# Kernel optimization log

Hardware: AMD Instinct MI355X
Metric: run time of the kernel (lower is better)

Reference implementation:

```python
import jax, jax.numpy as jnp
import numpy as np

B, T, W = 128, 256, 256
D, C, K = 128, 256, 12
TEMP = 0.1


def _l2norm(x):
    # matches F.normalize(dim=-1, eps=1e-12)
    return x / jnp.maximum(jnp.linalg.norm(x, axis=-1, keepdims=True), 1e-12)


def setup_inputs() -> dict:
    key = jax.random.key(0)
    ks = jax.random.split(key, 12)
    s = 0.02
    return {
        "rr_windows": jax.random.normal(ks[0], (B, T, W), dtype=jnp.float32),
        # Encoder: 2-layer MLP window->2D->D
        "enc_w1": jax.random.normal(ks[1], (W, 2 * D), dtype=jnp.float32) * s,
        "enc_b1": jnp.zeros((2 * D,), dtype=jnp.float32),
        "enc_w2": jax.random.normal(ks[2], (2 * D, D), dtype=jnp.float32) * s,
        "enc_b2": jnp.zeros((D,), dtype=jnp.float32),
        # ARBlock: single-layer GRU latent->context
        "W_ih": jax.random.normal(ks[3], (3 * C, D), dtype=jnp.float32) * s,
        "W_hh": jax.random.normal(ks[4], (3 * C, C), dtype=jnp.float32) * s,
        "b_ih": jnp.zeros((3 * C,), dtype=jnp.float32),
        "b_hh": jnp.zeros((3 * C,), dtype=jnp.float32),
        # K prediction heads Wk: context->latent
        "Wk_w": jax.random.normal(ks[5], (K, C, D), dtype=jnp.float32) * s,
        "Wk_b": jnp.zeros((K, D), dtype=jnp.float32),
    }


def _gru(z_seq, W_ih, W_hh, b_ih, b_hh):
    # z_seq: [B, T, D] -> c_seq [B, T, C]
    gx = jnp.einsum("btd,gd->btg", z_seq, W_ih) + b_ih  # [B,T,3C]
    gx = jnp.swapaxes(gx, 0, 1)  # [T,B,3C]
    h0 = jnp.zeros((z_seq.shape[0], C), dtype=z_seq.dtype)

    def step(h, gx_t):
        gh = h @ W_hh.T + b_hh
        xr, xz, xn = jnp.split(gx_t, 3, axis=-1)
        hr, hz, hn = jnp.split(gh, 3, axis=-1)
        r = jax.nn.sigmoid(xr + hr)
        zg = jax.nn.sigmoid(xz + hz)
        n = jnp.tanh(xn + r * hn)
        h_new = (1.0 - zg) * n + zg * h
        return h_new, h_new

    _, hs = jax.lax.scan(step, h0, gx)  # [T,B,C]
    return jnp.swapaxes(hs, 0, 1)


def reference(rr_windows, enc_w1, enc_b1, enc_w2, enc_b2, W_ih, W_hh, b_ih, b_hh, Wk_w, Wk_b):
    # Encoder on each window (dropout inactive)
    h = jax.nn.relu(jnp.einsum("btw,wh->bth", rr_windows, enc_w1) + enc_b1)
    z_seq = jnp.einsum("bth,hd->btd", h, enc_w2) + enc_b2  # [B,T,D]
    z_seq = _l2norm(z_seq)
    c_seq = _gru(z_seq, W_ih, W_hh, b_ih, b_hh)  # [B,T,C]

    Tp = T - K
    c_used = c_seq[:, :Tp, :]  # [B,Tp,C]
    # all (t,k) predictions at once: [K,B,Tp,D]
    preds = _l2norm(jnp.einsum("btc,kcd->kbtd", c_used, Wk_w) + Wk_b[:, None, None, :])
    # logits over ALL timesteps; cat([pos, negs-excl-pos]) == full set reordered,
    # so cross_entropy = logsumexp(full) - pos_logit (logsumexp order-invariant)
    logits = jnp.einsum("kbtd,bsd->kbts", preds, z_seq) / TEMP  # [K,B,Tp,T]
    pos_idx = jnp.arange(Tp)[None, :] + jnp.arange(1, K + 1)[:, None]  # [K,Tp]
    pos_logit = jnp.take_along_axis(
        logits, pos_idx[:, None, :, None], axis=-1
    )[..., 0]  # [K,B,Tp]
    avg_loss = jnp.mean(jax.nn.logsumexp(logits, axis=-1) - pos_logit)

    # accuracy: positive beats all negatives (ties to positive, as in argmax w/ pos first)
    is_pos = jnp.arange(T)[None, None, None, :] == pos_idx[:, None, :, None]
    neg_max = jnp.max(jnp.where(is_pos, -jnp.inf, logits), axis=-1)
    avg_accuracy = jnp.mean((pos_logit >= neg_max).astype(jnp.float32)) * 100.0
    return (avg_loss, avg_accuracy, z_seq, c_seq)
```

## Files before the change

### kernel.cpp

```cpp
#include <hip/hip_runtime.h>
#include <stdint.h>


typedef _Float16 f16;
typedef __attribute__((ext_vector_type(2))) _Float16 f16x2;
typedef __attribute__((ext_vector_type(8))) _Float16 f16x8;
typedef __attribute__((ext_vector_type(4))) float f32x4;

__device__ __forceinline__ f16x2 u2h(unsigned int x) { return __builtin_bit_cast(f16x2, x); }
__device__ __forceinline__ float sigm_(float x) { return __builtin_amdgcn_rcpf(1.f + __expf(-x)); }
__device__ __forceinline__ float tanh_(float x) { return 1.f - 2.f * __builtin_amdgcn_rcpf(__expf(2.f * x) + 1.f); }

#define NTOT_LOSS 374784.0f

__global__ void k_prep(const float* __restrict__ w1, const float* __restrict__ w2,
                       const float* __restrict__ wih, const float* __restrict__ whh,
                       const float* __restrict__ wkw,
                       f16* __restrict__ w1T, f16* __restrict__ w2T, f16* __restrict__ wihF,
                       uint8_t* __restrict__ whhQ, float* __restrict__ wsc,
                       f16* __restrict__ wkT, float* __restrict__ accb) {
  const int stride = gridDim.x * blockDim.x;
  const int tid = blockIdx.x * blockDim.x + threadIdx.x;
  if (tid == 0) { accb[0] = 0.f; accb[1] = 0.f; }
  for (int i = tid; i < 65536; i += stride) { int n = i >> 8, k = i & 255; w1T[i] = (f16)w1[k * 256 + n]; }
  for (int i = tid; i < 32768; i += stride) { int n = i >> 8, k = i & 255; w2T[i] = (f16)w2[k * 128 + n]; }
  for (int i = tid; i < 98304; i += stride) wihF[i] = (f16)wih[i];
  if (tid < 768) {
    const float* row = whh + (size_t)tid * 256;
    float amax = 0.f;
    for (int k = 0; k < 256; ++k) amax = fmaxf(amax, fabsf(row[k]));
    const float s = fmaxf(amax, 1e-20f) / 127.f;
    const float rs = 127.f / fmaxf(amax, 1e-20f);
    wsc[tid] = s / 127.f;
    for (int jq = 0; jq < 16; ++jq) {
      uint32_t words[4];
      for (int w32 = 0; w32 < 4; ++w32) {
        uint32_t p = 0;
        for (int e = 0; e < 4; ++e) {
          const int k = jq * 16 + w32 * 4 + e;
          const int q = (int)rintf(row[k] * rs);
          p |= ((uint32_t)(uint8_t)(int8_t)q) << (8 * e);
        }
        words[w32] = p;
      }
      *(uint4*)(whhQ + ((size_t)jq * 768 + tid) * 16) =
          make_uint4(words[0], words[1], words[2], words[3]);
    }
  }
  for (int i = tid; i < 393216; i += stride) {
    int kk = i >> 15, rem = i & 32767, d = rem >> 8, c = rem & 255;
    wkT[i] = (f16)wkw[(kk << 15) + c * 128 + d];
  }
}

template <int KTOT, bool AF32, bool RELU>
__global__ __launch_bounds__(256) void k_gemm64(const void* __restrict__ Aptr,
                                                const f16* __restrict__ BT,
                                                const float* __restrict__ bias,
                                                f16* __restrict__ out, const int NT) {
  __shared__ __align__(16) f16 Al[64][40];
  __shared__ __align__(16) f16 Bl[64][40];
  const int m0 = blockIdx.x * 64;
  const int n0 = blockIdx.y * 64;
  const int t = threadIdx.x;
  const int w = t >> 6, l = t & 63, lr = l & 15, lg = l >> 4;
  const int arow = t >> 2, akq = (t & 3) * 8;
  f32x4 acc[4] = {};
  for (int ks = 0; ks < KTOT / 32; ++ks) {
    const int kc = ks * 32;
    __syncthreads();
    if constexpr (AF32) {
      const float* src = (const float*)Aptr + (size_t)(m0 + arow) * KTOT + kc + akq;
      float4 v0 = *(const float4*)src;
      float4 v1 = *(const float4*)(src + 4);
      f16x8 hv = {(f16)v0.x, (f16)v0.y, (f16)v0.z, (f16)v0.w,
                  (f16)v1.x, (f16)v1.y, (f16)v1.z, (f16)v1.w};
      *(f16x8*)&Al[arow][akq] = hv;
    } else {
      const f16* src = (const f16*)Aptr + (size_t)(m0 + arow) * KTOT + kc + akq;
      *(f16x8*)&Al[arow][akq] = *(const f16x8*)src;
    }
    *(f16x8*)&Bl[arow][akq] = *(const f16x8*)(BT + (size_t)(n0 + arow) * KTOT + kc + akq);
    __syncthreads();
    f16x8 af = *(const f16x8*)&Al[16 * w + lr][lg * 8];
#pragma unroll
    for (int nt = 0; nt < 4; ++nt) {
      f16x8 bf = *(const f16x8*)&Bl[nt * 16 + lr][lg * 8];
      acc[nt] = __builtin_amdgcn_mfma_f32_16x16x32_f16(af, bf, acc[nt], 0, 0, 0);
    }
  }
#pragma unroll
  for (int nt = 0; nt < 4; ++nt) {
    const int n = n0 + nt * 16 + lr;
    const float bb = bias[n];
#pragma unroll
    for (int r = 0; r < 4; ++r) {
      const int m = m0 + 16 * w + lg * 4 + r;
      float v = acc[nt][r] + bb;
      if (RELU) v = fmaxf(v, 0.f);
      out[(size_t)m * NT + n] = (f16)v;
    }
  }
}

__global__ __launch_bounds__(256) void k_enc2(const f16* __restrict__ A, const f16* __restrict__ BT,
                                              const float* __restrict__ bias,
                                              float* __restrict__ zf32, f16* __restrict__ zf16) {
  __shared__ __align__(16) f16 Al[64][40];
  __shared__ __align__(16) f16 Bl[128][40];
  const int m0 = blockIdx.x * 64;
  const int t = threadIdx.x;
  const int w = t >> 6, l = t & 63, lr = l & 15, lg = l >> 4;
  const int arow = t >> 2, akq = (t & 3) * 8;
  f32x4 acc[8] = {};
  for (int ks = 0; ks < 8; ++ks) {
    const int kc = ks * 32;
    __syncthreads();
    *(f16x8*)&Al[arow][akq] = *(const f16x8*)(A + (size_t)(m0 + arow) * 256 + kc + akq);
#pragma unroll
    for (int hh = 0; hh < 2; ++hh) {
      const int brow = arow + 64 * hh;
      *(f16x8*)&Bl[brow][akq] = *(const f16x8*)(BT + (size_t)brow * 256 + kc + akq);
    }
    __syncthreads();
    f16x8 af = *(const f16x8*)&Al[16 * w + lr][lg * 8];
#pragma unroll
    for (int nt = 0; nt < 8; ++nt) {
      f16x8 bf = *(const f16x8*)&Bl[nt * 16 + lr][lg * 8];
      acc[nt] = __builtin_amdgcn_mfma_f32_16x16x32_f16(af, bf, acc[nt], 0, 0, 0);
    }
  }
  float v[8][4];
#pragma unroll
  for (int nt = 0; nt < 8; ++nt) {
    const float bb = bias[nt * 16 + lr];
#pragma unroll
    for (int r = 0; r < 4; ++r) v[nt][r] = acc[nt][r] + bb;
  }
#pragma unroll
  for (int r = 0; r < 4; ++r) {
    float ss = 0.f;
#pragma unroll
    for (int nt = 0; nt < 8; ++nt) ss += v[nt][r] * v[nt][r];
    ss += __shfl_xor(ss, 1); ss += __shfl_xor(ss, 2); ss += __shfl_xor(ss, 4); ss += __shfl_xor(ss, 8);
    const float scl = 1.f / fmaxf(sqrtf(ss), 1e-12f);
    const int m = m0 + 16 * w + lg * 4 + r;
#pragma unroll
    for (int nt = 0; nt < 8; ++nt) {
      const int n = nt * 16 + lr;
      const float z = v[nt][r] * scl;
      zf32[(size_t)m * 128 + n] = z;
      zf16[(size_t)m * 128 + n] = (f16)z;
    }
  }
}

__global__ __launch_bounds__(768, 3) void k_gru(const f16* __restrict__ gx, const uint8_t* __restrict__ whhQ,
                                                const float* __restrict__ wsc, const float* __restrict__ bhh,
                                                float* __restrict__ cout, f16* __restrict__ cf16) {
  __shared__ __align__(16) uint32_t h8[2][64];
  __shared__ float rz[2][256];
  const int b = blockIdx.x;
  const int o = threadIdx.x;
  const int g = o >> 8;
  const int c = o & 255;
  const float sc = wsc[o];
  const float bh = bhh[o];
  if (o < 64) { h8[0][o] = 0u; }
  float h_own = 0.f;
  const f16* gxp = gx + (size_t)b * 256 * 768 + o;
  float* coutp = cout + (size_t)b * 256 * 256 + c;
  f16* cfp = cf16 + (size_t)b * 256 * 256 + c;
  const uint8_t* wbase = whhQ + (size_t)o * 16;
  __syncthreads();
#pragma unroll 1
  for (int tt = 0; tt < 256; ++tt) {
    const int cur = tt & 1;
    const float gxv = (float)gxp[tt * 768];
    int i0 = 0, i1 = 0, i2 = 0, i3 = 0;
    const uint4* hp = (const uint4*)(&h8[cur][0]);
#pragma unroll
    for (int jq = 0; jq < 16; ++jq) {
      const uint4 wq = *(const uint4*)(wbase + (size_t)jq * 12288);
      const uint4 hq = hp[jq];
      i0 = __builtin_amdgcn_sdot4((int)wq.x, (int)hq.x, i0, false);
      i1 = __builtin_amdgcn_sdot4((int)wq.y, (int)hq.y, i1, false);
      i2 = __builtin_amdgcn_sdot4((int)wq.z, (int)hq.z, i2, false);
      i3 = __builtin_amdgcn_sdot4((int)wq.w, (int)hq.w, i3, false);
    }
    const float dot = (float)((i0 + i1) + (i2 + i3)) * sc + bh;
    if (g < 2) rz[g][c] = sigm_(gxv + dot);
    __syncthreads();
    if (g == 2) {
      const float r = rz[0][c], zz = rz[1][c];
      const float n = tanh_(gxv + r * dot);
      const float hn = (1.f - zz) * n + zz * h_own;
      h_own = hn;
      const int qh = (int)rintf(hn * 127.f);
      ((uint8_t*)&h8[cur ^ 1][0])[c] = (uint8_t)(int8_t)qh;
      coutp[tt * 256] = hn;
      cfp[tt * 256] = (f16)hn;
    }
    __syncthreads();
  }
}

__global__ __launch_bounds__(256) void k_cpc(const f16* __restrict__ cf16, const f16* __restrict__ zf16,
                                             const f16* __restrict__ wkT, const float* __restrict__ wkb,
                                             float* __restrict__ accb) {
  __shared__ __align__(16) f16 SMc[64 * 264];
  __shared__ __align__(16) f16 PB[64 * 136];
  __shared__ float red[2];
  f16 (*Bl)[40] = (f16(*)[40])PB;
  f16 (*P)[136] = (f16(*)[136])PB;
  const int kk = blockIdx.x, tc = blockIdx.y, b = blockIdx.z;
  const int t0 = tc * 64;
  const int t = threadIdx.x;
  const int w = t >> 6, l = t & 63, lr = l & 15, lg = l >> 4;
  {
    const uint32_t* src = (const uint32_t*)(cf16 + ((size_t)b * 256 + t0) * 256);
    uint32_t* dst = (uint32_t*)SMc;
#pragma unroll
    for (int it = 0; it < 32; ++it) {
      const int idx = it * 256 + t, row = idx >> 7, cw = idx & 127;
      dst[row * 132 + cw] = src[row * 128 + cw];
    }
  }
  f32x4 acc[8] = {};
  for (int ks = 0; ks < 8; ++ks) {
    __syncthreads();
    {
      const uint32_t* bsrc = (const uint32_t*)(wkT + ((size_t)kk << 15));
      uint32_t* bd = (uint32_t*)PB;
#pragma unroll
      for (int it = 0; it < 8; ++it) {
        const int idx = it * 256 + t, row = idx >> 4, kw = idx & 15;
        bd[row * 20 + kw] = bsrc[row * 128 + ks * 16 + kw];
      }
    }
    __syncthreads();
    f16x8 af = *(const f16x8*)&SMc[(16 * w + lr) * 264 + ks * 32 + lg * 8];
#pragma unroll
    for (int nt = 0; nt < 8; ++nt) {
      f16x8 bf = *(const f16x8*)&Bl[nt * 16 + lr][lg * 8];
      acc[nt] = __builtin_amdgcn_mfma_f32_16x16x32_f16(af, bf, acc[nt], 0, 0, 0);
    }
  }
  __syncthreads();
  {
    float v[8][4];
#pragma unroll
    for (int nt = 0; nt < 8; ++nt) {
      const float bb = wkb[kk * 128 + nt * 16 + lr];
#pragma unroll
      for (int r = 0; r < 4; ++r) v[nt][r] = acc[nt][r] + bb;
    }
#pragma unroll
    for (int r = 0; r < 4; ++r) {
      float ss = 0.f;
#pragma unroll
      for (int nt = 0; nt < 8; ++nt) ss += v[nt][r] * v[nt][r];
      ss += __shfl_xor(ss, 1); ss += __shfl_xor(ss, 2); ss += __shfl_xor(ss, 4); ss += __shfl_xor(ss, 8);
      const float scl = 1.f / fmaxf(sqrtf(ss), 1e-12f);
#pragma unroll
      for (int nt = 0; nt < 8; ++nt)
        P[16 * w + lg * 4 + r][nt * 16 + lr] = (f16)(v[nt][r] * scl);
    }
  }
  __syncthreads();
  float m_run[4], s_run[4], pos_v[4], neg_m[4];
#pragma unroll
  for (int r = 0; r < 4; ++r) { m_run[r] = -1e30f; s_run[r] = 0.f; pos_v[r] = -1e30f; neg_m[r] = -1e30f; }
  for (int sc = 0; sc < 4; ++sc) {
    __syncthreads();
    {
      const uint32_t* zsrc = (const uint32_t*)(zf16 + ((size_t)b * 256 + sc * 64) * 128);
      uint32_t* zd = (uint32_t*)SMc;
#pragma unroll
      for (int it = 0; it < 16; ++it) {
        const int idx = it * 256 + t, row = idx >> 6, cw = idx & 63;
        zd[row * 68 + cw] = zsrc[row * 64 + cw];
      }
    }
    __syncthreads();
    f32x4 sa[4] = {};
#pragma unroll
    for (int ks = 0; ks < 4; ++ks) {
      f16x8 af = *(const f16x8*)&P[16 * w + lr][ks * 32 + lg * 8];
#pragma unroll
      for (int nt = 0; nt < 4; ++nt) {
        f16x8 bf = *(const f16x8*)&SMc[(nt * 16 + lr) * 136 + ks * 32 + lg * 8];
        sa[nt] = __builtin_amdgcn_mfma_f32_16x16x32_f16(af, bf, sa[nt], 0, 0, 0);
      }
    }
#pragma unroll
    for (int r = 0; r < 4; ++r) {
      const int trow = t0 + 16 * w + lg * 4 + r;
      const int pos_s = trow + kk + 1;
      float vv[4];
#pragma unroll
      for (int nt = 0; nt < 4; ++nt) vv[nt] = sa[nt][r] * 10.f;
      float cm = fmaxf(fmaxf(vv[0], vv[1]), fmaxf(vv[2], vv[3]));
      cm = fmaxf(cm, __shfl_xor(cm, 1)); cm = fmaxf(cm, __shfl_xor(cm, 2));
      cm = fmaxf(cm, __shfl_xor(cm, 4)); cm = fmaxf(cm, __shfl_xor(cm, 8));
      const float nm = fmaxf(m_run[r], cm);
      float ps = __expf(vv[0] - nm) + __expf(vv[1] - nm) + __expf(vv[2] - nm) + __expf(vv[3] - nm);
      ps += __shfl_xor(ps, 1); ps += __shfl_xor(ps, 2); ps += __shfl_xor(ps, 4); ps += __shfl_xor(ps, 8);
      s_run[r] = s_run[r] * __expf(m_run[r] - nm) + ps;
      m_run[r] = nm;
      const int sbase = sc * 64 + lr;
#pragma unroll
      for (int nt = 0; nt < 4; ++nt) {
        const int s = sbase + nt * 16;
        if (s == pos_s) pos_v[r] = vv[nt];
        else neg_m[r] = fmaxf(neg_m[r], vv[nt]);
      }
    }
  }
  __syncthreads();
  if (t == 0) { red[0] = 0.f; red[1] = 0.f; }
  __syncthreads();
  float lsum = 0.f, csum = 0.f;
#pragma unroll
  for (int r = 0; r < 4; ++r) {
    float pv = pos_v[r], ng = neg_m[r];
    pv = fmaxf(pv, __shfl_xor(pv, 1)); pv = fmaxf(pv, __shfl_xor(pv, 2));
    pv = fmaxf(pv, __shfl_xor(pv, 4)); pv = fmaxf(pv, __shfl_xor(pv, 8));
    ng = fmaxf(ng, __shfl_xor(ng, 1)); ng = fmaxf(ng, __shfl_xor(ng, 2));
    ng = fmaxf(ng, __shfl_xor(ng, 4)); ng = fmaxf(ng, __shfl_xor(ng, 8));
    const int trow = t0 + 16 * w + lg * 4 + r;
    if (lr == 0 && trow < 244) {
      const float lse = m_run[r] + __logf(s_run[r]);
      lsum += lse - pv;
      csum += (pv >= ng) ? 1.f : 0.f;
    }
  }
  if (lr == 0) { atomicAdd(&red[0], lsum); atomicAdd(&red[1], csum); }
  __syncthreads();
  if (t == 0) { atomicAdd(&accb[0], red[0]); atomicAdd(&accb[1], red[1]); }
}

__global__ void k_fin(const float* __restrict__ accb, float* __restrict__ out) {
  out[0] = accb[0] * (1.0f / NTOT_LOSS);
  out[1] = accb[1] * (100.0f / NTOT_LOSS);
}

extern "C" void kernel_launch(void* const* d_in, const int* in_sizes, int n_in,
                              void* d_out, int out_size, void* d_ws, size_t ws_size,
                              hipStream_t stream) {
  (void)in_sizes; (void)n_in; (void)out_size; (void)ws_size;
  const float* rr  = (const float*)d_in[0];
  const float* w1  = (const float*)d_in[1];
  const float* b1  = (const float*)d_in[2];
  const float* w2  = (const float*)d_in[3];
  const float* b2  = (const float*)d_in[4];
  const float* wih = (const float*)d_in[5];
  const float* whh = (const float*)d_in[6];
  const float* bih = (const float*)d_in[7];
  const float* bhh = (const float*)d_in[8];
  const float* wkw = (const float*)d_in[9];
  const float* wkb = (const float*)d_in[10];
  float* out = (float*)d_out;
  char* ws = (char*)d_ws;

  const size_t GX_B = (size_t)32768 * 768 * 2;
  f16* gx   = (f16*)ws;
  f16* h1   = (f16*)ws;
  f16* zf16 = (f16*)(ws + GX_B);
  f16* cf16 = (f16*)(ws + GX_B + 8388608);
  f16* w1T  = (f16*)(ws + GX_B + 8388608 + 16777216);
  f16* w2T  = w1T + 65536;
  f16* wihF = w2T + 32768;
  uint8_t* whhQ = (uint8_t*)(wihF + 98304);
  float* wsc = (float*)(whhQ + 196608);
  f16* wkT  = (f16*)(wsc + 768);
  float* accb = (float*)(wkT + 393216);

  float* zf32 = out + 2;
  float* cf32 = out + 2 + 4194304;

  k_prep<<<256, 256, 0, stream>>>(w1, w2, wih, whh, wkw, w1T, w2T, wihF, whhQ, wsc, wkT, accb);
  k_gemm64<256, true, true><<<dim3(512, 4), 256, 0, stream>>>(rr, w1T, b1, h1, 256);
  k_enc2<<<dim3(512), 256, 0, stream>>>(h1, w2T, b2, zf32, zf16);
  k_gemm64<128, false, false><<<dim3(512, 12), 256, 0, stream>>>(zf16, wihF, bih, gx, 768);
  k_gru<<<128, 768, 0, stream>>>(gx, whhQ, wsc, bhh, cf32, cf16);
  k_cpc<<<dim3(12, 4, 128), 256, 0, stream>>>(cf16, zf16, wkT, wkb, accb);
  k_fin<<<1, 1, 0, stream>>>(accb, out);
}
```

Before: 485.9 us.

## Restructure CPC kernel: direct global A loads, per-wave s-split, cross-wave LSE merge

The CPC loss kernel no longer stages the context tile in shared memory. A-fragments are read straight from global memory, and the Wk tile is loaded in two wide chunks instead of eight narrow ones, which cuts barriers. In the logits phase each wave now owns a slice of the s dimension with z as the A operand. It keeps per-column online softmax state and merges it across lanes and across waves through a small shared buffer, replacing the per-block shared atomics. This lowers LDS footprint and sync count, at the cost of uncoalesced-ish global fragment loads and an extra cross-wave combine.

```diff
diff --git a/kernel.cpp b/kernel.cpp
--- a/kernel.cpp
+++ b/kernel.cpp
@@ -29,9 +29,8 @@
     const float* row = whh + (size_t)tid * 256;
     float amax = 0.f;
     for (int k = 0; k < 256; ++k) amax = fmaxf(amax, fabsf(row[k]));
-    const float s = fmaxf(amax, 1e-20f) / 127.f;
     const float rs = 127.f / fmaxf(amax, 1e-20f);
-    wsc[tid] = s / 127.f;
+    wsc[tid] = fmaxf(amax, 1e-20f) / (127.f * 127.f);
     for (int jq = 0; jq < 16; ++jq) {
       uint32_t words[4];
       for (int w32 = 0; w32 < 4; ++w32) {
@@ -208,42 +207,37 @@
 __global__ __launch_bounds__(256) void k_cpc(const f16* __restrict__ cf16, const f16* __restrict__ zf16,
                                              const f16* __restrict__ wkT, const float* __restrict__ wkb,
                                              float* __restrict__ accb) {
-  __shared__ __align__(16) f16 SMc[64 * 264];
-  __shared__ __align__(16) f16 PB[64 * 136];
-  __shared__ float red[2];
-  f16 (*Bl)[40] = (f16(*)[40])PB;
-  f16 (*P)[136] = (f16(*)[136])PB;
+  __shared__ __align__(16) char PB[34816];
+  f16* Blp = (f16*)PB;
+  f16* Pp = (f16*)PB;
+  float4* comb = (float4*)(PB + 17408);
   const int kk = blockIdx.x, tc = blockIdx.y, b = blockIdx.z;
   const int t0 = tc * 64;
   const int t = threadIdx.x;
-  const int w = t >> 6, l = t & 63, lr = l & 15, lg = l >> 4;
-  {
-    const uint32_t* src = (const uint32_t*)(cf16 + ((size_t)b * 256 + t0) * 256);
-    uint32_t* dst = (uint32_t*)SMc;
-#pragma unroll
-    for (int it = 0; it < 32; ++it) {
-      const int idx = it * 256 + t, row = idx >> 7, cw = idx & 127;
-      dst[row * 132 + cw] = src[row * 128 + cw];
-    }
-  }
+  const int w = t >> 6, l = t & 63, lr = l & 15, hi = l >> 4;
   f32x4 acc[8] = {};
-  for (int ks = 0; ks < 8; ++ks) {
+  const f16* cbase = cf16 + ((size_t)b * 256 + t0 + 16 * w + lr) * 256;
+#pragma unroll 1
+  for (int p = 0; p < 2; ++p) {
     __syncthreads();
     {
-      const uint32_t* bsrc = (const uint32_t*)(wkT + ((size_t)kk << 15));
+      const uint32_t* bsrc = (const uint32_t*)(wkT + ((size_t)kk << 15)) + p * 64;
       uint32_t* bd = (uint32_t*)PB;
 #pragma unroll
-      for (int it = 0; it < 8; ++it) {
-        const int idx = it * 256 + t, row = idx >> 4, kw = idx & 15;
-        bd[row * 20 + kw] = bsrc[row * 128 + ks * 16 + kw];
-      }
-    }
-    __syncthreads();
-    f16x8 af = *(const f16x8*)&SMc[(16 * w + lr) * 264 + ks * 32 + lg * 8];
-#pragma unroll
-    for (int nt = 0; nt < 8; ++nt) {
-      f16x8 bf = *(const f16x8*)&Bl[nt * 16 + lr][lg * 8];
-      acc[nt] = __builtin_amdgcn_mfma_f32_16x16x32_f16(af, bf, acc[nt], 0, 0, 0);
+      for (int it = 0; it < 32; ++it) {
+        const int idx = it * 256 + t, row = idx >> 6, cw = idx & 63;
+        bd[row * 68 + cw] = bsrc[row * 128 + cw];
+      }
+    }
+    __syncthreads();
+#pragma unroll
+    for (int ks = 0; ks < 4; ++ks) {
+      const f16x8 af = *(const f16x8*)(cbase + p * 128 + ks * 32 + hi * 8);
+#pragma unroll
+      for (int nt = 0; nt < 8; ++nt) {
+        const f16x8 bf = *(const f16x8*)(Blp + (nt * 16 + lr) * 136 + ks * 32 + hi * 8);
+        acc[nt] = __builtin_amdgcn_mfma_f32_16x16x32_f16(af, bf, acc[nt], 0, 0, 0);
+      }
     }
   }
   __syncthreads();
@@ -264,80 +258,89 @@
       const float scl = 1.f / fmaxf(sqrtf(ss), 1e-12f);
 #pragma unroll
       for (int nt = 0; nt < 8; ++nt)
-        P[16 * w + lg * 4 + r][nt * 16 + lr] = (f16)(v[nt][r] * scl);
+        Pp[(16 * w + hi * 4 + r) * 136 + nt * 16 + lr] = (f16)(v[nt][r] * scl);
     }
   }
   __syncthreads();
-  float m_run[4], s_run[4], pos_v[4], neg_m[4];
-#pragma unroll
-  for (int r = 0; r < 4; ++r) { m_run[r] = -1e30f; s_run[r] = 0.f; pos_v[r] = -1e30f; neg_m[r] = -1e30f; }
-  for (int sc = 0; sc < 4; ++sc) {
-    __syncthreads();
-    {
-      const uint32_t* zsrc = (const uint32_t*)(zf16 + ((size_t)b * 256 + sc * 64) * 128);
-      uint32_t* zd = (uint32_t*)SMc;
-#pragma unroll
-      for (int it = 0; it < 16; ++it) {
-        const int idx = it * 256 + t, row = idx >> 6, cw = idx & 63;
-        zd[row * 68 + cw] = zsrc[row * 64 + cw];
-      }
-    }
-    __syncthreads();
-    f32x4 sa[4] = {};
-#pragma unroll
-    for (int ks = 0; ks < 4; ++ks) {
-      f16x8 af = *(const f16x8*)&P[16 * w + lr][ks * 32 + lg * 8];
-#pragma unroll
-      for (int nt = 0; nt < 4; ++nt) {
-        f16x8 bf = *(const f16x8*)&SMc[(nt * 16 + lr) * 136 + ks * 32 + lg * 8];
-        sa[nt] = __builtin_amdgcn_mfma_f32_16x16x32_f16(af, bf, sa[nt], 0, 0, 0);
-      }
-    }
-#pragma unroll
-    for (int r = 0; r < 4; ++r) {
-      const int trow = t0 + 16 * w + lg * 4 + r;
-      const int pos_s = trow + kk + 1;
+  float m_[4], l_[4], pos_[4], neg_[4];
+#pragma unroll
+  for (int nt = 0; nt < 4; ++nt) { m_[nt] = -1e30f; l_[nt] = 0.f; pos_[nt] = -1e30f; neg_[nt] = -1e30f; }
+  const f16* zbase = zf16 + (size_t)b * 32768;
+#pragma unroll 1
+  for (int stile = 0; stile < 4; ++stile) {
+    const int sb = 64 * w + 16 * stile;
+    f16x8 af[4];
+#pragma unroll
+    for (int ks = 0; ks < 4; ++ks)
+      af[ks] = *(const f16x8*)(zbase + (size_t)(sb + lr) * 128 + ks * 32 + hi * 8);
+#pragma unroll
+    for (int nt = 0; nt < 4; ++nt) {
+      f32x4 sa = {};
+#pragma unroll
+      for (int ks = 0; ks < 4; ++ks) {
+        const f16x8 bf = *(const f16x8*)(Pp + (nt * 16 + lr) * 136 + ks * 32 + hi * 8);
+        sa = __builtin_amdgcn_mfma_f32_16x16x32_f16(af[ks], bf, sa, 0, 0, 0);
+      }
+      const int pos_s = t0 + nt * 16 + lr + kk + 1;
       float vv[4];
 #pragma unroll
-      for (int nt = 0; nt < 4; ++nt) vv[nt] = sa[nt][r] * 10.f;
-      float cm = fmaxf(fmaxf(vv[0], vv[1]), fmaxf(vv[2], vv[3]));
-      cm = fmaxf(cm, __shfl_xor(cm, 1)); cm = fmaxf(cm, __shfl_xor(cm, 2));
-      cm = fmaxf(cm, __shfl_xor(cm, 4)); cm = fmaxf(cm, __shfl_xor(cm, 8));
-      const float nm = fmaxf(m_run[r], cm);
-      float ps = __expf(vv[0] - nm) + __expf(vv[1] - nm) + __expf(vv[2] - nm) + __expf(vv[3] - nm);
-      ps += __shfl_xor(ps, 1); ps += __shfl_xor(ps, 2); ps += __shfl_xor(ps, 4); ps += __shfl_xor(ps, 8);
-      s_run[r] = s_run[r] * __expf(m_run[r] - nm) + ps;
-      m_run[r] = nm;
-      const int sbase = sc * 64 + lr;
-#pragma unroll
-      for (int nt = 0; nt < 4; ++nt) {
-        const int s = sbase + nt * 16;
-        if (s == pos_s) pos_v[r] = vv[nt];
-        else neg_m[r] = fmaxf(neg_m[r], vv[nt]);
-      }
-    }
+      for (int r = 0; r < 4; ++r) vv[r] = sa[r] * 10.f;
+      const float cm = fmaxf(fmaxf(vv[0], vv[1]), fmaxf(vv[2], vv[3]));
+      const float nm = fmaxf(m_[nt], cm);
+      const float ps = __expf(vv[0] - nm) + __expf(vv[1] - nm) +
+                       __expf(vv[2] - nm) + __expf(vv[3] - nm);
+      l_[nt] = l_[nt] * __expf(m_[nt] - nm) + ps;
+      m_[nt] = nm;
+#pragma unroll
+      for (int r = 0; r < 4; ++r) {
+        const int s = sb + 4 * hi + r;
+        if (s == pos_s) pos_[nt] = vv[r];
+        else neg_[nt] = fmaxf(neg_[nt], vv[r]);
+      }
+    }
+  }
+#pragma unroll
+  for (int nt = 0; nt < 4; ++nt) {
+#pragma unroll
+    for (int d = 16; d <= 32; d <<= 1) {
+      const float mo = __shfl_xor(m_[nt], d);
+      const float lo = __shfl_xor(l_[nt], d);
+      const float po = __shfl_xor(pos_[nt], d);
+      const float no = __shfl_xor(neg_[nt], d);
+      const float nm = fmaxf(m_[nt], mo);
+      l_[nt] = l_[nt] * __expf(m_[nt] - nm) + lo * __expf(mo - nm);
+      m_[nt] = nm;
+      pos_[nt] = fmaxf(pos_[nt], po);
+      neg_[nt] = fmaxf(neg_[nt], no);
+    }
+    if (l < 16) comb[w * 64 + nt * 16 + lr] = make_float4(m_[nt], l_[nt], pos_[nt], neg_[nt]);
   }
   __syncthreads();
-  if (t == 0) { red[0] = 0.f; red[1] = 0.f; }
-  __syncthreads();
-  float lsum = 0.f, csum = 0.f;
-#pragma unroll
-  for (int r = 0; r < 4; ++r) {
-    float pv = pos_v[r], ng = neg_m[r];
-    pv = fmaxf(pv, __shfl_xor(pv, 1)); pv = fmaxf(pv, __shfl_xor(pv, 2));
-    pv = fmaxf(pv, __shfl_xor(pv, 4)); pv = fmaxf(pv, __shfl_xor(pv, 8));
-    ng = fmaxf(ng, __shfl_xor(ng, 1)); ng = fmaxf(ng, __shfl_xor(ng, 2));
-    ng = fmaxf(ng, __shfl_xor(ng, 4)); ng = fmaxf(ng, __shfl_xor(ng, 8));
-    const int trow = t0 + 16 * w + lg * 4 + r;
-    if (lr == 0 && trow < 244) {
-      const float lse = m_run[r] + __logf(s_run[r]);
-      lsum += lse - pv;
-      csum += (pv >= ng) ? 1.f : 0.f;
-    }
-  }
-  if (lr == 0) { atomicAdd(&red[0], lsum); atomicAdd(&red[1], csum); }
-  __syncthreads();
-  if (t == 0) { atomicAdd(&accb[0], red[0]); atomicAdd(&accb[1], red[1]); }
+  if (t < 64) {
+    float M = -1e30f, L = 0.f, PV = -1e30f, NG = -1e30f;
+#pragma unroll
+    for (int ws = 0; ws < 4; ++ws) {
+      const float4 v = comb[ws * 64 + t];
+      const float nm = fmaxf(M, v.x);
+      L = L * __expf(M - nm) + v.y * __expf(v.x - nm);
+      M = nm;
+      PV = fmaxf(PV, v.z);
+      NG = fmaxf(NG, v.w);
+    }
+    float lsum = 0.f, csum = 0.f;
+    const int trow = t0 + t;
+    if (trow < 244) {
+      lsum = (M + __logf(L)) - PV;
+      csum = (PV >= NG) ? 1.f : 0.f;
+    }
+    lsum += __shfl_xor(lsum, 1); csum += __shfl_xor(csum, 1);
+    lsum += __shfl_xor(lsum, 2); csum += __shfl_xor(csum, 2);
+    lsum += __shfl_xor(lsum, 4); csum += __shfl_xor(csum, 4);
+    lsum += __shfl_xor(lsum, 8); csum += __shfl_xor(csum, 8);
+    lsum += __shfl_xor(lsum, 16); csum += __shfl_xor(csum, 16);
+    lsum += __shfl_xor(lsum, 32); csum += __shfl_xor(csum, 32);
+    if (t == 0) { atomicAdd(&accb[0], lsum); atomicAdd(&accb[1], csum); }
+  }
 }
 
 __global__ void k_fin(const float* __restrict__ accb, float* __restrict__ out) {
```

After: 517.8 us. +6.6%, slower.
